# Kernel tuning notes

Hardware: AMD Instinct MI355X
Metric: run time of the kernel (lower is better)

The kernel has to match this reference:

```python
import jax, jax.numpy as jnp
import numpy as np

BATCH = 131072
NUM_OSC = 4
NUM_SPEC = 300
FREQ_LO, FREQ_HI = 0.5, 5.0


def setup_inputs() -> dict:
    key = jax.random.key(0)
    ks = jax.random.split(key, 8)
    return {
        "G": jax.random.normal(ks[0], (BATCH, 8), dtype=jnp.float32),
        "W1": jax.random.normal(ks[1], (100, 8), dtype=jnp.float32) * 0.3,
        "b1": jax.random.normal(ks[2], (100,), dtype=jnp.float32) * 0.1,
        "W2": jax.random.normal(ks[3], (100, 100), dtype=jnp.float32) * 0.1,
        "b2": jax.random.normal(ks[4], (100,), dtype=jnp.float32) * 0.1,
        "W_w0": jax.random.normal(ks[5], (NUM_OSC, 100), dtype=jnp.float32) * 0.1,
        "W_wp": jax.random.normal(ks[6], (NUM_OSC, 100), dtype=jnp.float32) * 0.1,
        # torch.nn.init.uniform_(lin_g.weight, a=0.0, b=0.1)
        "W_g": jax.random.uniform(ks[7], (NUM_OSC, 100), dtype=jnp.float32) * 0.1,
    }


def reference(G, W1, b1, W2, b2, W_w0, W_wp, W_g):
    # MLP trunk: 8 -> 100 -> 100, ReLU on both layers
    out = jax.nn.relu(G @ W1.T + b1)
    out = jax.nn.relu(out @ W2.T + b2)          # (B, 100)

    # Oscillator parameter heads (bias-free), ReLU-clamped, shape (B, 4, 1)
    w0 = jax.nn.relu(out @ W_w0.T)[:, :, None]
    wp = jax.nn.relu(out @ W_wp.T)[:, :, None]
    g = jax.nn.relu(out @ W_g.T)[:, :, None]

    # Frequency grid (300,) broadcast against (B, 4, 1)
    w = jnp.arange(FREQ_LO, FREQ_HI, (FREQ_HI - FREQ_LO) / NUM_SPEC, dtype=jnp.float32)

    # Lorentz oscillator imaginary permittivity
    num = (wp ** 2) * (w * g)                   # (B, 4, 300)
    den = (w0 ** 2 - w ** 2) ** 2 + (w ** 2) * (g ** 2)
    e2 = num / den
    return jnp.sum(e2, axis=1)                  # (B, 300)
```

## Files before the change

### kernel.cpp

```cpp
#include <hip/hip_runtime.h>

#define BATCH 131072
#define NS    300
#define H     100
#define BLK   256
#define EPB   256
#define NQ4   (EPB * NS / 4)

#define REP25(M) M(0) M(1) M(2) M(3) M(4) M(5) M(6) M(7) M(8) M(9) M(10) M(11) \
  M(12) M(13) M(14) M(15) M(16) M(17) M(18) M(19) M(20) M(21) M(22) M(23) M(24)

__device__ __forceinline__ float qswap1(float x) {
    return __int_as_float(__builtin_amdgcn_mov_dpp(__float_as_int(x), 0xB1, 0xF, 0xF, true));
}
__device__ __forceinline__ float qswap2(float x) {
    return __int_as_float(__builtin_amdgcn_mov_dpp(__float_as_int(x), 0x4E, 0xF, 0xF, true));
}

__global__ __launch_bounds__(BLK, 2)
void lorentz_fused(const float* __restrict__ G,  const float* __restrict__ W1,
                   const float* __restrict__ b1, const float* __restrict__ W2,
                   const float* __restrict__ b2, const float* __restrict__ Ww0,
                   const float* __restrict__ Wwp, const float* __restrict__ Wg,
                   float* __restrict__ out)
{
    __shared__ float4 sW2c4[H * 4 * 7];
    __shared__ float4 sHead4[H * 4];
    __shared__ float4 sP04[EPB], sP14[EPB], sP24[EPB];
    __shared__ float  sW1[H * 8];
    __shared__ float  sB1[H], sB2[H];

    const int tid = threadIdx.x;

    {
        float* sW2cF = (float*)sW2c4;
        for (int i = tid; i < H * H; i += BLK) {
            int j = i / 100, k = i - j * 100;
            int q = k / 25, kk = k - q * 25;
            sW2cF[(j * 4 + q) * 28 + kk] = W2[i];
        }
        for (int i = tid; i < H * 8; i += BLK) sW1[i] = W1[i];
        for (int i = tid; i < H; i += BLK) { sB1[i] = b1[i]; sB2[i] = b2[i]; }
        float* sHeadF = (float*)sHead4;
        for (int i = tid; i < H * 4; i += BLK) {
            int j = i >> 2, q = i & 3;
            sHeadF[i * 4 + 0] = Ww0[q * H + j];
            sHeadF[i * 4 + 1] = Wwp[q * H + j];
            sHeadF[i * 4 + 2] = Wg [q * H + j];
            sHeadF[i * 4 + 3] = 0.f;
        }
    }
    __syncthreads();

    const int q  = tid & 3;
    const int gi = tid >> 2;
    const int e0 = blockIdx.x * EPB + gi * 4;

    const float4* gp = (const float4*)(G + (size_t)e0 * 8);
    const float4 ga0 = gp[0], gb0 = gp[1];
    const float4 ga1 = gp[2], gb1 = gp[3];
    const float4 ga2 = gp[4], gb2 = gp[5];
    const float4 ga3 = gp[6], gb3 = gp[7];

#define H1DECL(i) float h1a_##i, h1b_##i, h1c_##i, h1d_##i;
    REP25(H1DECL)
#undef H1DECL
#define L1E(dst, ga, gb)                                                        \
        { float s0 = fmaf(ga.x, ra.x, bb);  float s1 = ga.y * ra.y;             \
          s0 = fmaf(ga.z, ra.z, s0);  s1 = fmaf(ga.w, ra.w, s1);                \
          s0 = fmaf(gb.x, rb.x, s0);  s1 = fmaf(gb.y, rb.y, s1);                \
          s0 = fmaf(gb.z, rb.z, s0);  s1 = fmaf(gb.w, rb.w, s1);                \
          dst = fmaxf(s0 + s1, 0.f); }
#define L1(i) { const float4* r = (const float4*)&sW1[(q * 25 + (i)) * 8];      \
        const float4 ra = r[0], rb = r[1];                                      \
        const float bb = sB1[q * 25 + (i)];                                     \
        L1E(h1a_##i, ga0, gb0)  L1E(h1b_##i, ga1, gb1)                          \
        L1E(h1c_##i, ga2, gb2)  L1E(h1d_##i, ga3, gb3) }
    REP25(L1)
#undef L1

    float aw0a = 0.f, awpa = 0.f, agga = 0.f;
    float aw0b = 0.f, awpb = 0.f, aggb = 0.f;
    float aw0c = 0.f, awpc = 0.f, aggc = 0.f;
    float aw0d = 0.f, awpd = 0.f, aggd = 0.f;

#pragma unroll 2
    for (int j = 0; j < H; ++j) {
        const int cb = (j * 4 + q) * 7;
        const float4 c0 = sW2c4[cb + 0], c1 = sW2c4[cb + 1], c2 = sW2c4[cb + 2],
                     c3 = sW2c4[cb + 3], c4 = sW2c4[cb + 4], c5 = sW2c4[cb + 5],
                     c6 = sW2c4[cb + 6];
        const float4 hv  = sHead4[j * 4 + q];
        const float  b2j = sB2[j];

        float pa = 0.f, pb = 0.f, pc = 0.f, pd = 0.f;
#define CH1(w, i)                                                               \
        pa = fmaf(h1a_##i, w, pa); pb = fmaf(h1b_##i, w, pb);                   \
        pc = fmaf(h1c_##i, w, pc); pd = fmaf(h1d_##i, w, pd);
#define CH(t, i0, i1, i2, i3)                                                   \
        CH1(c##t.x, i0) CH1(c##t.y, i1) CH1(c##t.z, i2) CH1(c##t.w, i3)
        CH(0, 0, 1, 2, 3)     CH(1, 4, 5, 6, 7)     CH(2, 8, 9, 10, 11)
        CH(3, 12, 13, 14, 15) CH(4, 16, 17, 18, 19) CH(5, 20, 21, 22, 23)
        CH1(c6.x, 24)
#undef CH
#undef CH1
        float sa = pa + qswap1(pa); sa += qswap2(sa);
        float sb = pb + qswap1(pb); sb += qswap2(sb);
        float sc = pc + qswap1(pc); sc += qswap2(sc);
        float sd = pd + qswap1(pd); sd += qswap2(sd);
        const float h2a = fmaxf(sa + b2j, 0.f);
        const float h2b = fmaxf(sb + b2j, 0.f);
        const float h2c = fmaxf(sc + b2j, 0.f);
        const float h2d = fmaxf(sd + b2j, 0.f);

        aw0a = fmaf(h2a, hv.x, aw0a); awpa = fmaf(h2a, hv.y, awpa); agga = fmaf(h2a, hv.z, agga);
        aw0b = fmaf(h2b, hv.x, aw0b); awpb = fmaf(h2b, hv.y, awpb); aggb = fmaf(h2b, hv.z, aggb);
        aw0c = fmaf(h2c, hv.x, aw0c); awpc = fmaf(h2c, hv.y, awpc); aggc = fmaf(h2c, hv.z, aggc);
        aw0d = fmaf(h2d, hv.x, aw0d); awpd = fmaf(h2d, hv.y, awpd); aggd = fmaf(h2d, hv.z, aggd);
    }

    {
        float* P0 = (float*)sP04; float* P1 = (float*)sP14; float* P2 = (float*)sP24;
#define EMIT(aw, ap, ag, e)                                                     \
        { const float w0 = fmaxf(aw, 0.f), wp = fmaxf(ap, 0.f), gg = fmaxf(ag, 0.f); \
          const int ix = (gi * 4 + (e)) * 4 + q;                                \
          P0[ix] = w0 * w0;  P1[ix] = gg * gg;  P2[ix] = wp * wp * gg; }
        EMIT(aw0a, awpa, agga, 0)
        EMIT(aw0b, awpb, aggb, 1)
        EMIT(aw0c, awpc, aggc, 2)
        EMIT(aw0d, awpd, aggd, 3)
#undef EMIT
    }
    __syncthreads();

    float4* out4 = (float4*)out;
    const size_t base4 = (size_t)blockIdx.x * NQ4;

    for (int it = 0; it < NQ4 / BLK; ++it) {
        const int idx4 = it * BLK + tid;
        const int e  = idx4 / 75;
        const int k4 = idx4 - e * 75;
        const float4 P0 = sP04[e], P1 = sP14[e], P2 = sP24[e];
        const float kb = (float)(k4 << 2);
        float4 r; float* rp = (float*)&r;
#pragma unroll
        for (int i = 0; i < 4; ++i) {
            const float w   = 0.5f + (kb + (float)i) * 0.015f;
            const float wsq = w * w;
            const float t0 = P0.x - wsq, t1 = P0.y - wsq,
                        t2 = P0.z - wsq, t3 = P0.w - wsq;
            const float d0 = fmaf(t0, t0, wsq * P1.x);
            const float d1 = fmaf(t1, t1, wsq * P1.y);
            const float d2 = fmaf(t2, t2, wsq * P1.z);
            const float d3 = fmaf(t3, t3, wsq * P1.w);
            const float d01 = d0 * d1, d23 = d2 * d3;
            const float D   = d01 * d23;
            const float n01 = fmaf(P2.y, d0, P2.x * d1);
            const float n23 = fmaf(P2.w, d2, P2.z * d3);
            const float N   = fmaf(n01, d23, n23 * d01);
            rp[i] = w * (N * __builtin_amdgcn_rcpf(D));
        }
        out4[base4 + idx4] = r;
    }
}

extern "C" void kernel_launch(void* const* d_in, const int* in_sizes, int n_in,
                              void* d_out, int out_size, void* d_ws, size_t ws_size,
                              hipStream_t stream) {
    const float* G   = (const float*)d_in[0];
    const float* W1  = (const float*)d_in[1];
    const float* b1  = (const float*)d_in[2];
    const float* W2  = (const float*)d_in[3];
    const float* b2  = (const float*)d_in[4];
    const float* Ww0 = (const float*)d_in[5];
    const float* Wwp = (const float*)d_in[6];
    const float* Wg  = (const float*)d_in[7];
    float* out = (float*)d_out;

    dim3 grid(BATCH / EPB);
    dim3 block(BLK);
    lorentz_fused<<<grid, block, 0, stream>>>(G, W1, b1, W2, b2, Ww0, Wwp, Wg, out);
}
```

Measured before the change: 81.74 us.

## Double block size and halve per-thread elements to cut register pressure

```diff
diff --git a/kernel.cpp b/kernel.cpp
--- a/kernel.cpp
+++ b/kernel.cpp
@@ -3,7 +3,7 @@
 #define BATCH 131072
 #define NS    300
 #define H     100
-#define BLK   256
+#define BLK   512
 #define EPB   256
 #define NQ4   (EPB * NS / 4)
 
@@ -17,7 +17,7 @@
     return __int_as_float(__builtin_amdgcn_mov_dpp(__float_as_int(x), 0x4E, 0xF, 0xF, true));
 }
 
-__global__ __launch_bounds__(BLK, 2)
+__global__ __launch_bounds__(BLK, 4)
 void lorentz_fused(const float* __restrict__ G,  const float* __restrict__ W1,
                    const float* __restrict__ b1, const float* __restrict__ W2,
                    const float* __restrict__ b2, const float* __restrict__ Ww0,
@@ -54,15 +54,13 @@
 
     const int q  = tid & 3;
     const int gi = tid >> 2;
-    const int e0 = blockIdx.x * EPB + gi * 4;
+    const int e0 = blockIdx.x * EPB + gi * 2;
 
     const float4* gp = (const float4*)(G + (size_t)e0 * 8);
     const float4 ga0 = gp[0], gb0 = gp[1];
     const float4 ga1 = gp[2], gb1 = gp[3];
-    const float4 ga2 = gp[4], gb2 = gp[5];
-    const float4 ga3 = gp[6], gb3 = gp[7];
 
-#define H1DECL(i) float h1a_##i, h1b_##i, h1c_##i, h1d_##i;
+#define H1DECL(i) float h1a_##i, h1b_##i;
     REP25(H1DECL)
 #undef H1DECL
 #define L1E(dst, ga, gb)                                                        \
@@ -74,15 +72,12 @@
 #define L1(i) { const float4* r = (const float4*)&sW1[(q * 25 + (i)) * 8];      \
         const float4 ra = r[0], rb = r[1];                                      \
         const float bb = sB1[q * 25 + (i)];                                     \
-        L1E(h1a_##i, ga0, gb0)  L1E(h1b_##i, ga1, gb1)                          \
-        L1E(h1c_##i, ga2, gb2)  L1E(h1d_##i, ga3, gb3) }
+        L1E(h1a_##i, ga0, gb0)  L1E(h1b_##i, ga1, gb1) }
     REP25(L1)
 #undef L1
 
     float aw0a = 0.f, awpa = 0.f, agga = 0.f;
     float aw0b = 0.f, awpb = 0.f, aggb = 0.f;
-    float aw0c = 0.f, awpc = 0.f, aggc = 0.f;
-    float aw0d = 0.f, awpd = 0.f, aggd = 0.f;
 
 #pragma unroll 2
     for (int j = 0; j < H; ++j) {
@@ -93,10 +88,8 @@
         const float4 hv  = sHead4[j * 4 + q];
         const float  b2j = sB2[j];
 
-        float pa = 0.f, pb = 0.f, pc = 0.f, pd = 0.f;
-#define CH1(w, i)                                                               \
-        pa = fmaf(h1a_##i, w, pa); pb = fmaf(h1b_##i, w, pb);                   \
-        pc = fmaf(h1c_##i, w, pc); pd = fmaf(h1d_##i, w, pd);
+        float pa = 0.f, pb = 0.f;
+#define CH1(w, i) pa = fmaf(h1a_##i, w, pa); pb = fmaf(h1b_##i, w, pb);
 #define CH(t, i0, i1, i2, i3)                                                   \
         CH1(c##t.x, i0) CH1(c##t.y, i1) CH1(c##t.z, i2) CH1(c##t.w, i3)
         CH(0, 0, 1, 2, 3)     CH(1, 4, 5, 6, 7)     CH(2, 8, 9, 10, 11)
@@ -106,29 +99,21 @@
 #undef CH1
         float sa = pa + qswap1(pa); sa += qswap2(sa);
         float sb = pb + qswap1(pb); sb += qswap2(sb);
-        float sc = pc + qswap1(pc); sc += qswap2(sc);
-        float sd = pd + qswap1(pd); sd += qswap2(sd);
         const float h2a = fmaxf(sa + b2j, 0.f);
         const float h2b = fmaxf(sb + b2j, 0.f);
-        const float h2c = fmaxf(sc + b2j, 0.f);
-        const float h2d = fmaxf(sd + b2j, 0.f);
 
         aw0a = fmaf(h2a, hv.x, aw0a); awpa = fmaf(h2a, hv.y, awpa); agga = fmaf(h2a, hv.z, agga);
         aw0b = fmaf(h2b, hv.x, aw0b); awpb = fmaf(h2b, hv.y, awpb); aggb = fmaf(h2b, hv.z, aggb);
-        aw0c = fmaf(h2c, hv.x, aw0c); awpc = fmaf(h2c, hv.y, awpc); aggc = fmaf(h2c, hv.z, aggc);
-        aw0d = fmaf(h2d, hv.x, aw0d); awpd = fmaf(h2d, hv.y, awpd); aggd = fmaf(h2d, hv.z, aggd);
     }
 
     {
         float* P0 = (float*)sP04; float* P1 = (float*)sP14; float* P2 = (float*)sP24;
 #define EMIT(aw, ap, ag, e)                                                     \
         { const float w0 = fmaxf(aw, 0.f), wp = fmaxf(ap, 0.f), gg = fmaxf(ag, 0.f); \
-          const int ix = (gi * 4 + (e)) * 4 + q;                                \
+          const int ix = (gi * 2 + (e)) * 4 + q;                                \
           P0[ix] = w0 * w0;  P1[ix] = gg * gg;  P2[ix] = wp * wp * gg; }
         EMIT(aw0a, awpa, agga, 0)
         EMIT(aw0b, awpb, aggb, 1)
-        EMIT(aw0c, awpc, aggc, 2)
-        EMIT(aw0d, awpd, aggd, 3)
 #undef EMIT
     }
     __syncthreads();
@@ -136,32 +121,40 @@
     float4* out4 = (float4*)out;
     const size_t base4 = (size_t)blockIdx.x * NQ4;
 
+#define SPEC(idx4)                                                              \
+    {   const int e  = (idx4) / 75;                                             \
+        const int k4 = (idx4) - e * 75;                                         \
+        const float4 P0 = sP04[e], P1 = sP14[e], P2 = sP24[e];                  \
+        const float kb = (float)(k4 << 2);                                      \
+        float4 r; float* rp = (float*)&r;                                       \
+        _Pragma("unroll")                                                       \
+        for (int i = 0; i < 4; ++i) {                                           \
+            const float w   = 0.5f + (kb + (float)i) * 0.015f;                  \
+            const float wsq = w * w;                                            \
+            const float t0 = P0.x - wsq, t1 = P0.y - wsq,                       \
+                        t2 = P0.z - wsq, t3 = P0.w - wsq;                       \
+            const float d0 = fmaf(t0, t0, wsq * P1.x);                          \
+            const float d1 = fmaf(t1, t1, wsq * P1.y);                          \
+            const float d2 = fmaf(t2, t2, wsq * P1.z);                          \
+            const float d3 = fmaf(t3, t3, wsq * P1.w);                          \
+            const float d01 = d0 * d1, d23 = d2 * d3;                           \
+            const float D   = d01 * d23;                                        \
+            const float n01 = fmaf(P2.y, d0, P2.x * d1);                        \
+            const float n23 = fmaf(P2.w, d2, P2.z * d3);                        \
+            const float N   = fmaf(n01, d23, n23 * d01);                        \
+            rp[i] = w * (N * __builtin_amdgcn_rcpf(D));                         \
+        }                                                                       \
+        out4[base4 + (idx4)] = r; }
+
     for (int it = 0; it < NQ4 / BLK; ++it) {
         const int idx4 = it * BLK + tid;
-        const int e  = idx4 / 75;
-        const int k4 = idx4 - e * 75;
-        const float4 P0 = sP04[e], P1 = sP14[e], P2 = sP24[e];
-        const float kb = (float)(k4 << 2);
-        float4 r; float* rp = (float*)&r;
-#pragma unroll
-        for (int i = 0; i < 4; ++i) {
-            const float w   = 0.5f + (kb + (float)i) * 0.015f;
-            const float wsq = w * w;
-            const float t0 = P0.x - wsq, t1 = P0.y - wsq,
-                        t2 = P0.z - wsq, t3 = P0.w - wsq;
-            const float d0 = fmaf(t0, t0, wsq * P1.x);
-            const float d1 = fmaf(t1, t1, wsq * P1.y);
-            const float d2 = fmaf(t2, t2, wsq * P1.z);
-            const float d3 = fmaf(t3, t3, wsq * P1.w);
-            const float d01 = d0 * d1, d23 = d2 * d3;
-            const float D   = d01 * d23;
-            const float n01 = fmaf(P2.y, d0, P2.x * d1);
-            const float n23 = fmaf(P2.w, d2, P2.z * d3);
-            const float N   = fmaf(n01, d23, n23 * d01);
-            rp[i] = w * (N * __builtin_amdgcn_rcpf(D));
-        }
-        out4[base4 + idx4] = r;
+        SPEC(idx4)
     }
+    if (tid < NQ4 - (NQ4 / BLK) * BLK) {
+        const int idx4 = (NQ4 / BLK) * BLK + tid;
+        SPEC(idx4)
+    }
+#undef SPEC
 }
 
 extern "C" void kernel_launch(void* const* d_in, const int* in_sizes, int n_in,
```

New measurement: 83.73 us. +2.4%, slower.
